# Performance work log

Hardware: AMD Instinct MI355X
Metric: run time of the kernel (lower is better)

The kernel has to match this reference:

```python
import jax, jax.numpy as jnp
import numpy as np

B, H, W = 64, 256, 256
G = 64
V = G * G          # 4096
HID = 512
S = 50


def _conv(x, w, b):
    # x: (B,C,H,W), w: (O,I,3,3) -> 'same' conv, NCHW
    y = jax.lax.conv_general_dilated(x, w, (1, 1), 'SAME',
                                     dimension_numbers=('NCHW', 'OIHW', 'NCHW'))
    return y + b[None, :, None, None]


def setup_inputs() -> dict:
    key = jax.random.key(0)
    ks = jax.random.split(key, 14)

    def lin(k, shape, fan_in):
        return (jax.random.normal(k, shape, jnp.float32) / np.float32(np.sqrt(fan_in)))

    return {
        'mask': jax.random.uniform(ks[0], (B, 1, H, W), jnp.float32),
        'target_ids': jax.random.randint(ks[1], (B, S), 0, V),
        'conv1_w': lin(ks[2], (16, 1, 3, 3), 9), 'conv1_b': jnp.zeros((16,), jnp.float32),
        'conv2_w': lin(ks[3], (32, 16, 3, 3), 16 * 9), 'conv2_b': jnp.zeros((32,), jnp.float32),
        'feat_w': lin(ks[4], (HID, 32), 32), 'feat_b': jnp.zeros((HID,), jnp.float32),
        'ctx_w': lin(ks[5], (HID, HID), HID), 'ctx_b': jnp.zeros((HID,), jnp.float32),
        'tok_emb': jax.random.normal(ks[6], (V + 1, HID), jnp.float32) * 0.02,
        'w_ih': lin(ks[7], (4 * HID, HID), HID), 'w_hh': lin(ks[8], (4 * HID, HID), HID),
        'b_ih': jnp.zeros((4 * HID,), jnp.float32), 'b_hh': jnp.zeros((4 * HID,), jnp.float32),
        'head_w': lin(ks[9], (V, HID), HID), 'head_b': jnp.zeros((V,), jnp.float32),
    }


def reference(mask, target_ids, conv1_w, conv1_b, conv2_w, conv2_b,
              feat_w, feat_b, ctx_w, ctx_b, tok_emb,
              w_ih, w_hh, b_ih, b_hh, head_w, head_b):
    b = mask.shape[0]
    vocab = head_w.shape[0]

    # --- CNN encoder ---
    x = jax.nn.relu(_conv(mask, conv1_w, conv1_b))                    # (B,16,H,W)
    x = jax.lax.reduce_window(x, -jnp.inf, jax.lax.max,
                              (1, 1, 2, 2), (1, 1, 2, 2), 'VALID')    # (B,16,H/2,W/2)
    x = jax.nn.relu(_conv(x, conv2_w, conv2_b))                       # (B,32,H/2,W/2)
    x = x.mean(axis=(2, 3))                                           # AdaptiveAvgPool2d(1) -> (B,32)

    h0 = x @ feat_w.T + feat_b                                        # (B,HID)
    c0 = jnp.zeros_like(h0)
    ctx = h0 @ ctx_w.T + ctx_b                                        # (B,HID)

    # Full teacher forcing (ratio=1.0): input token at t=0 is start token V,
    # at t>0 it is target_ids[:, t-1]. All embeddings gathered upfront.
    start = jnp.full((b, 1), vocab, dtype=target_ids.dtype)
    toks = jnp.concatenate([start, target_ids[:, :-1]], axis=1)       # (B,S)
    embs = tok_emb[toks]                                              # (B,S,HID)
    lstm_in = jnp.swapaxes(embs, 0, 1) + ctx[None]                    # (S,B,HID)

    bias = b_ih + b_hh

    def step(carry, inp):
        h, c = carry
        gates = inp @ w_ih.T + h @ w_hh.T + bias                      # (B,4*HID)
        i, f, g, o = jnp.split(gates, 4, axis=-1)
        c = jax.nn.sigmoid(f) * c + jax.nn.sigmoid(i) * jnp.tanh(g)
        h = jax.nn.sigmoid(o) * jnp.tanh(c)
        logit = h @ head_w.T + head_b                                 # (B,V)
        return (h, c), logit

    _, logits = jax.lax.scan(step, (h0, c0), lstm_in)                 # (S,B,V)
    return jnp.swapaxes(logits, 0, 1)                                 # (B,S,V)
```

## Files before the change

kernel.cpp:

```cpp
#include <hip/hip_runtime.h>
#include <cmath>

typedef __attribute__((ext_vector_type(8))) _Float16 f16x8;
typedef __attribute__((ext_vector_type(4))) float f32x4;
typedef __attribute__((ext_vector_type(4))) unsigned u32x4;

#define LSTM_NB 32

__device__ __forceinline__ unsigned short f2h(float x) {
  return __builtin_bit_cast(unsigned short, (_Float16)x);
}

__device__ __forceinline__ void gload16(const void* g, void* l) {
  __builtin_amdgcn_global_load_lds(
      (const __attribute__((address_space(1))) void*)g,
      (__attribute__((address_space(3))) void*)l, 16, 0, 0);
}

__device__ __forceinline__ void cload16(const void* p, u32x4* dst) {
  asm volatile("global_load_dwordx4 %0, %1, off sc0 sc1"
               : "=v"(*dst)
               : "v"(p));
}

__global__ __launch_bounds__(512) void k_conv(
    const float* __restrict__ mask, const float* __restrict__ w1,
    const float* __restrict__ b1, const float* __restrict__ w2,
    const float* __restrict__ b2, float* __restrict__ part)
{
  __shared__ float s_p1[16][18 * 36];
  __shared__ float s_w1[144];
  __shared__ float s_b1[16];
  __shared__ float s_w2[4608];
  __shared__ float s_b2[32];

  const int tid = threadIdx.x;
  const int b = blockIdx.x >> 5;
  const int tile = blockIdx.x & 31;
  const int px0 = (tile & 3) * 32, py0 = (tile >> 2) * 16;
  const float* mb = mask + (size_t)b * 65536;

  for (int i = tid; i < 144; i += 512) s_w1[i] = w1[i];
  for (int i = tid; i < 4608; i += 512) s_w2[i] = w2[i];
  if (tid < 16) s_b1[tid] = b1[tid];
  if (tid < 32) s_b2[tid] = b2[tid];
  __syncthreads();

  for (int idx = tid; idx < 18 * 34; idx += 512) {
    int ly = idx / 34, lx = idx - ly * 34;
    int py = py0 - 1 + ly, px = px0 - 1 + lx;
    if (py < 0 || py >= 128 || px < 0 || px >= 128) {
      for (int o = 0; o < 16; o++) s_p1[o][ly * 36 + lx] = 0.f;
    } else {
      float patch[4][4];
      int gy0 = 2 * py - 1, gx0 = 2 * px - 1;
#pragma unroll
      for (int i = 0; i < 4; i++) {
        int gy = gy0 + i;
        bool yok = (gy >= 0 && gy < 256);
#pragma unroll
        for (int j = 0; j < 4; j++) {
          int gx = gx0 + j;
          patch[i][j] = (yok && gx >= 0 && gx < 256) ? mb[gy * 256 + gx] : 0.f;
        }
      }
      for (int o = 0; o < 16; o++) {
        float m = 0.f;
#pragma unroll
        for (int dy = 0; dy < 2; dy++)
#pragma unroll
          for (int dx = 0; dx < 2; dx++) {
            float v = s_b1[o];
#pragma unroll
            for (int ky = 0; ky < 3; ky++)
#pragma unroll
              for (int kx = 0; kx < 3; kx++)
                v = fmaf(patch[dy + ky][dx + kx], s_w1[o * 9 + ky * 3 + kx], v);
            m = fmaxf(m, v);
          }
        s_p1[o][ly * 36 + lx] = m;
      }
    }
  }
  __syncthreads();

  const int ocg = tid >> 6;
  const int sp = tid & 63;
  const int sx = (sp & 7) * 4, sy = (sp >> 3) * 2;
  float acc[4][8];
#pragma unroll
  for (int a = 0; a < 4; a++)
#pragma unroll
    for (int q = 0; q < 8; q++) acc[a][q] = 0.f;

  for (int ic = 0; ic < 16; ic++) {
    float p[4][6];
#pragma unroll
    for (int i = 0; i < 4; i++) {
      const float* row = &s_p1[ic][(sy + i) * 36 + sx];
#pragma unroll
      for (int j = 0; j < 6; j++) p[i][j] = row[j];
    }
#pragma unroll
    for (int o4 = 0; o4 < 4; o4++) {
      const int oc = ocg * 4 + o4;
      const float* w = &s_w2[(oc * 16 + ic) * 9];
      float w00 = w[0], w01 = w[1], w02 = w[2];
      float w10 = w[3], w11 = w[4], w12 = w[5];
      float w20 = w[6], w21 = w[7], w22 = w[8];
#pragma unroll
      for (int y = 0; y < 2; y++)
#pragma unroll
        for (int x = 0; x < 4; x++) {
          float s = acc[o4][y * 4 + x];
          s = fmaf(p[y][x], w00, s);
          s = fmaf(p[y][x + 1], w01, s);
          s = fmaf(p[y][x + 2], w02, s);
          s = fmaf(p[y + 1][x], w10, s);
          s = fmaf(p[y + 1][x + 1], w11, s);
          s = fmaf(p[y + 1][x + 2], w12, s);
          s = fmaf(p[y + 2][x], w20, s);
          s = fmaf(p[y + 2][x + 1], w21, s);
          s = fmaf(p[y + 2][x + 2], w22, s);
          acc[o4][y * 4 + x] = s;
        }
    }
  }

  const int lane = tid & 63;
#pragma unroll
  for (int o4 = 0; o4 < 4; o4++) {
    float bv = s_b2[ocg * 4 + o4];
    float s = 0.f;
#pragma unroll
    for (int q = 0; q < 8; q++) s += fmaxf(acc[o4][q] + bv, 0.f);
    for (int off = 32; off > 0; off >>= 1) s += __shfl_down(s, off, 64);
    if (lane == 0) part[(b * 32 + tile) * 32 + ocg * 4 + o4] = s;
  }
}

__global__ __launch_bounds__(256) void k_pool_h0(
    const float* __restrict__ part, const float* __restrict__ feat_w,
    const float* __restrict__ feat_b, float* __restrict__ h0,
    unsigned short* __restrict__ h0f)
{
  const int b = blockIdx.x, tid = threadIdx.x;
  __shared__ float pl[32];
  if (tid < 32) {
    float s = 0.f;
    for (int t = 0; t < 32; t++) s += part[(b * 32 + t) * 32 + tid];
    pl[tid] = s * (1.0f / 16384.0f);
  }
  __syncthreads();
  for (int j = tid; j < 512; j += 256) {
    float acc = feat_b[j];
    const float* w = feat_w + j * 32;
#pragma unroll
    for (int ic = 0; ic < 32; ic++) acc = fmaf(pl[ic], w[ic], acc);
    h0[b * 512 + j] = acc;
    h0f[b * 512 + j] = f2h(acc);
  }
}

__global__ __launch_bounds__(256) void k_ctx(
    const float* __restrict__ h0, const float* __restrict__ ctx_w,
    const float* __restrict__ ctx_b, float* __restrict__ ctx)
{
  const int b = blockIdx.x, tid = threadIdx.x;
  __shared__ float hs[512];
  for (int k = tid; k < 512; k += 256) hs[k] = h0[b * 512 + k];
  __syncthreads();
  for (int j = tid; j < 512; j += 256) {
    const float* w = ctx_w + (size_t)j * 512;
    float s0 = 0.f, s1 = 0.f, s2 = 0.f, s3 = 0.f;
    for (int k = 0; k < 512; k += 4) {
      float4 w4 = *(const float4*)(w + k);
      s0 = fmaf(hs[k], w4.x, s0);
      s1 = fmaf(hs[k + 1], w4.y, s1);
      s2 = fmaf(hs[k + 2], w4.z, s2);
      s3 = fmaf(hs[k + 3], w4.w, s3);
    }
    ctx[b * 512 + j] = ctx_b[j] + ((s0 + s1) + (s2 + s3));
  }
}

__global__ __launch_bounds__(256) void k_f2h(
    const float* __restrict__ in, unsigned short* __restrict__ out, int n)
{
  int i = (blockIdx.x * 256 + threadIdx.x) * 4;
  if (i < n) {
    float4 v = *(const float4*)(in + i);
    unsigned lo = (unsigned)f2h(v.x) | ((unsigned)f2h(v.y) << 16);
    unsigned hi = (unsigned)f2h(v.z) | ((unsigned)f2h(v.w) << 16);
    *(uint2*)(out + i) = make_uint2(lo, hi);
  }
}

__global__ __launch_bounds__(64) void k_zero(int* __restrict__ p) {
  p[threadIdx.x] = 0;
}
__global__ __launch_bounds__(256) void k_zero_f(float* __restrict__ p) {
  p[blockIdx.x * 256 + threadIdx.x] = 0.f;
}

__global__ __launch_bounds__(128) void k_build_A(
    const float* __restrict__ tok_emb, const int* __restrict__ tgt,
    const float* __restrict__ ctx, unsigned short* __restrict__ A)
{
  const int r = blockIdx.x;
  const int t = r >> 6, b = r & 63;
  const int tok = (t == 0) ? 4096 : tgt[b * 50 + (t - 1)];
  const int i = threadIdx.x * 4;
  float4 ev = *(const float4*)(tok_emb + (size_t)tok * 512 + i);
  float4 cv = *(const float4*)(ctx + b * 512 + i);
  unsigned lo = (unsigned)f2h(ev.x + cv.x) | ((unsigned)f2h(ev.y + cv.y) << 16);
  unsigned hi = (unsigned)f2h(ev.z + cv.z) | ((unsigned)f2h(ev.w + cv.w) << 16);
  *(uint2*)(A + (size_t)r * 512 + i) = make_uint2(lo, hi);
}

template <int MODE>
__global__ __launch_bounds__(256) void k_gemm_mfma(
    const unsigned short* __restrict__ A, const unsigned short* __restrict__ B,
    const float* __restrict__ bias_a, const float* __restrict__ bias_b,
    float* __restrict__ C, int NB)
{
  __shared__ unsigned short sA[128 * 32];
  __shared__ unsigned short sB[128 * 32];
  const int tid = threadIdx.x;
  const int bx = blockIdx.x % NB, by = blockIdx.x / NB;
  const int lane = tid & 63, wv = tid >> 6;
  const int wr = wv >> 1, wc = wv & 1;
  const unsigned short* Ab = A + (size_t)by * 128 * 512;
  const unsigned short* Bb = B + (size_t)bx * 128 * 512;

  f32x4 acc[4][4];
#pragma unroll
  for (int m = 0; m < 4; m++)
#pragma unroll
    for (int n = 0; n < 4; n++) acc[m][n] = (f32x4){0.f, 0.f, 0.f, 0.f};

  const int r0 = tid >> 2, c0 = (tid & 3) * 8;
  const int idx1 = tid + 256;
  const int r1 = idx1 >> 2, c1 = (idx1 & 3) * 8;
  unsigned short* lA0 = sA + (size_t)wv * 512;
  unsigned short* lA1 = sA + 2048 + (size_t)wv * 512;
  unsigned short* lB0 = sB + (size_t)wv * 512;
  unsigned short* lB1 = sB + 2048 + (size_t)wv * 512;

  const int frow = lane & 15;
  const int foff = (lane >> 4) * 8;

  for (int kc = 0; kc < 512; kc += 32) {
    gload16(Ab + (size_t)r0 * 512 + kc + c0, lA0);
    gload16(Ab + (size_t)r1 * 512 + kc + c1, lA1);
    gload16(Bb + (size_t)r0 * 512 + kc + c0, lB0);
    gload16(Bb + (size_t)r1 * 512 + kc + c1, lB1);
    __syncthreads();

    f16x8 af[4], bfr[4];
#pragma unroll
    for (int m = 0; m < 4; m++)
      af[m] = *(const f16x8*)(sA + (wr * 64 + m * 16 + frow) * 32 + foff);
#pragma unroll
    for (int n = 0; n < 4; n++)
      bfr[n] = *(const f16x8*)(sB + (wc * 64 + n * 16 + frow) * 32 + foff);
#pragma unroll
    for (int m = 0; m < 4; m++)
#pragma unroll
      for (int n = 0; n < 4; n++)
        acc[m][n] = __builtin_amdgcn_mfma_f32_16x16x32_f16(
            af[m], bfr[n], acc[m][n], 0, 0, 0);
    __syncthreads();
  }

#pragma unroll
  for (int n = 0; n < 4; n++) {
    const int gc = bx * 128 + wc * 64 + n * 16 + (lane & 15);
    const float bv = (MODE == 0) ? (bias_a[gc] + bias_b[gc]) : bias_a[gc];
#pragma unroll
    for (int m = 0; m < 4; m++) {
      const int rb = by * 128 + wr * 64 + m * 16 + (lane >> 4) * 4;
#pragma unroll
      for (int j = 0; j < 4; j++) {
        const int r = rb + j;
        float v = acc[m][n][j] + bv;
        int t = r >> 6, bb = r & 63;
        if (MODE == 0) {
          C[(size_t)t * 131072 + (size_t)gc * 64 + bb] = v;
        } else {
          C[((size_t)bb * 50 + t) * 4096 + gc] = v;
        }
      }
    }
  }
}

__global__ __launch_bounds__(256, 1) void k_lstm_mfma(
    const float* __restrict__ xgT,
    const float* __restrict__ w_hh,
    const unsigned short* __restrict__ h0f,
    unsigned short* __restrict__ hallf,
    int* __restrict__ cnt)
{
  __shared__ unsigned short s_h[64 * 512];
  __shared__ float s_g[4][64][17];
  const int tid = threadIdx.x;
  const int kb = blockIdx.x;
  const int g = tid >> 6;
  const int lane = tid & 63;
  const int frow = lane & 15;
  const int foff = (lane >> 4) * 8;

  f16x8 wf[16];
  {
    const float* wrow = w_hh + (size_t)(g * 512 + kb * 16 + frow) * 512;
#pragma unroll
    for (int kf = 0; kf < 16; kf++) {
      float tmp[8];
      *(float4*)tmp = *(const float4*)(wrow + kf * 32 + foff);
      *(float4*)(tmp + 4) = *(const float4*)(wrow + kf * 32 + foff + 4);
#pragma unroll
      for (int j = 0; j < 8; j++) wf[kf][j] = (_Float16)tmp[j];
    }
  }

  float c[4] = {0.f, 0.f, 0.f, 0.f};
  const int b2 = tid & 63, dd2 = tid >> 6;

  for (int t = 0; t < 50; ++t) {
    const unsigned short* H = t ? hallf + (size_t)(t - 1) * 32768 : h0f;

    const float* xr =
        xgT + (size_t)t * 131072 + (size_t)(kb * 16 + dd2 * 4) * 64 + b2;
    float xv[16];
#pragma unroll
    for (int gq = 0; gq < 4; gq++)
#pragma unroll
      for (int i = 0; i < 4; i++)
        xv[gq * 4 + i] = xr[(size_t)(gq * 512 + i) * 64];

    {
      u32x4 r[16];
#pragma unroll
      for (int i = 0; i < 16; i++)
        cload16((const char*)H + (size_t)(tid + i * 256) * 16, &r[i]);
      asm volatile("s_waitcnt vmcnt(0)" ::: "memory");
      __builtin_amdgcn_sched_barrier(0);
#pragma unroll
      for (int i = 0; i < 16; i++) {
        int byte = (tid + i * 256) * 16;
        int swz = byte ^ (((byte >> 10) & 7) << 4);
        *(u32x4*)((char*)s_h + swz) = r[i];
      }
    }
    __syncthreads();

    f32x4 acc[4];
#pragma unroll
    for (int mt = 0; mt < 4; mt++) acc[mt] = (f32x4){0.f, 0.f, 0.f, 0.f};
#pragma unroll
    for (int kf = 0; kf < 16; kf++) {
#pragma unroll
      for (int mt = 0; mt < 4; mt++) {
        const int row = mt * 16 + frow;
        const int byte = (row << 10) + kf * 64 + foff * 2;
        const int swz = byte ^ ((row & 7) << 4);
        f16x8 ah = *(const f16x8*)((const char*)s_h + swz);
        acc[mt] =
            __builtin_amdgcn_mfma_f32_16x16x32_f16(ah, wf[kf], acc[mt], 0, 0, 0);
      }
    }
#pragma unroll
    for (int mt = 0; mt < 4; mt++)
#pragma unroll
      for (int j = 0; j < 4; j++)
        s_g[g][mt * 16 + (lane >> 4) * 4 + j][frow] = acc[mt][j];
    __syncthreads();

    unsigned long long qf = 0;
#pragma unroll
    for (int i = 0; i < 4; i++) {
      float gi = s_g[0][b2][dd2 * 4 + i] + xv[0 + i];
      float gf = s_g[1][b2][dd2 * 4 + i] + xv[4 + i];
      float gg = s_g[2][b2][dd2 * 4 + i] + xv[8 + i];
      float go = s_g[3][b2][dd2 * 4 + i] + xv[12 + i];
      float ig = 1.f / (1.f + expf(-gi));
      float fg = 1.f / (1.f + expf(-gf));
      float og = 1.f / (1.f + expf(-go));
      float gt = tanhf(gg);
      c[i] = fmaf(fg, c[i], ig * gt);
      float h = og * tanhf(c[i]);
      qf |= (unsigned long long)f2h(h) << (16 * i);
    }
    const size_t ho = (size_t)b2 * 512 + kb * 16 + dd2 * 4;
    __hip_atomic_store((unsigned long long*)(hallf + (size_t)t * 32768 + ho),
                       qf, __ATOMIC_RELAXED, __HIP_MEMORY_SCOPE_AGENT);
    __syncthreads();
    if (tid == 0) {
      __hip_atomic_fetch_add(&cnt[t], 1, __ATOMIC_RELAXED,
                             __HIP_MEMORY_SCOPE_AGENT);
      while (__hip_atomic_load(&cnt[t], __ATOMIC_RELAXED,
                               __HIP_MEMORY_SCOPE_AGENT) < LSTM_NB) {
        __builtin_amdgcn_s_sleep(1);
      }
    }
    __syncthreads();
  }
}

__global__ __launch_bounds__(256) void k_lstm_step1(
    const float* __restrict__ xgT, const float* __restrict__ w_hh,
    const float* __restrict__ hin, float* __restrict__ hout,
    unsigned short* __restrict__ hallf_t, float* __restrict__ cbuf, int t)
{
  __shared__ float s_w[8][512];
  __shared__ float s_g[2][4][64];
  const int tid = threadIdx.x;
  const int dd0 = blockIdx.x * 2;

  for (int idx = tid; idx < 1024; idx += 256) {
    int row = idx >> 7;
    int k4 = (idx & 127) << 2;
    int q_ = row >> 1, dd_i = row & 1;
    *(float4*)&s_w[row][k4] =
        *(const float4*)(w_hh + (size_t)(q_ * 512 + dd0 + dd_i) * 512 + k4);
  }
  const int b = tid & 63;
  const int q = tid >> 6;
  __syncthreads();

  const float* hc = hin + b * 512;
  const float* xr = xgT + (size_t)t * 131072 + (size_t)(q * 512 + dd0) * 64 + b;
  float a0 = xr[0], a1 = xr[64];
  const float* w0 = s_w[q * 2 + 0];
  const float* w1 = s_w[q * 2 + 1];
#pragma unroll 8
  for (int k = 0; k < 512; k += 4) {
    float4 h4 = *(const float4*)(hc + k);
    float4 u = *(const float4*)(w0 + k);
    float4 v = *(const float4*)(w1 + k);
    a0 = fmaf(h4.x, u.x, fmaf(h4.y, u.y, fmaf(h4.z, u.z, fmaf(h4.w, u.w, a0))));
    a1 = fmaf(h4.x, v.x, fmaf(h4.y, v.y, fmaf(h4.z, v.z, fmaf(h4.w, v.w, a1))));
  }
  s_g[0][q][b] = a0;
  s_g[1][q][b] = a1;
  __syncthreads();
  if (q < 2) {
    const int dd = dd0 + q;
    float gi = s_g[q][0][b], gf = s_g[q][1][b];
    float gg = s_g[q][2][b], go = s_g[q][3][b];
    float ig = 1.f / (1.f + expf(-gi));
    float fg = 1.f / (1.f + expf(-gf));
    float og = 1.f / (1.f + expf(-go));
    float gt = tanhf(gg);
    float c = fmaf(fg, cbuf[b * 512 + dd], ig * gt);
    float h = og * tanhf(c);
    cbuf[b * 512 + dd] = c;
    hout[b * 512 + dd] = h;
    hallf_t[(size_t)b * 512 + dd] = f2h(h);
  }
}

extern "C" void kernel_launch(void* const* d_in, const int* in_sizes, int n_in,
                              void* d_out, int out_size, void* d_ws,
                              size_t ws_size, hipStream_t stream) {
  const float* mask   = (const float*)d_in[0];
  const int*   tgt    = (const int*)d_in[1];
  const float* w1     = (const float*)d_in[2];
  const float* b1     = (const float*)d_in[3];
  const float* w2     = (const float*)d_in[4];
  const float* b2     = (const float*)d_in[5];
  const float* feat_w = (const float*)d_in[6];
  const float* feat_b = (const float*)d_in[7];
  const float* ctx_w  = (const float*)d_in[8];
  const float* ctx_b  = (const float*)d_in[9];
  const float* temb   = (const float*)d_in[10];
  const float* w_ih   = (const float*)d_in[11];
  const float* w_hh_p = (const float*)d_in[12];
  const float* b_ih   = (const float*)d_in[13];
  const float* b_hh   = (const float*)d_in[14];
  const float* head_w = (const float*)d_in[15];
  const float* head_b = (const float*)d_in[16];

  float* ws = (float*)d_ws;
  float* part  = ws;
  float* hbuf  = ws + 65536;
  float* ctx   = ws + 131072;
  int*   cnt   = (int*)(ws + 163840);
  unsigned short* h0f  = (unsigned short*)(ws + 163904);
  unsigned short* Ab16 = (unsigned short*)(ws + 180288);
  unsigned short* hallf = Ab16;
  unsigned short* wihb = (unsigned short*)(ws + 999488);
  unsigned short* hwb  = (unsigned short*)(ws + 1523776);
  float* xgT   = ws + 2572352;
  float* cbuf  = part;
  float* out   = (float*)d_out;

  k_conv<<<2048, 512, 0, stream>>>(mask, w1, b1, w2, b2, part);
  k_f2h<<<1024, 256, 0, stream>>>(w_ih, wihb, 1048576);
  k_f2h<<<2048, 256, 0, stream>>>(head_w, hwb, 2097152);
  k_zero<<<1, 64, 0, stream>>>(cnt);
  k_pool_h0<<<64, 256, 0, stream>>>(part, feat_w, feat_b, hbuf, h0f);
  k_ctx<<<64, 256, 0, stream>>>(hbuf, ctx_w, ctx_b, ctx);
  k_build_A<<<3200, 128, 0, stream>>>(temb, tgt, ctx, Ab16);
  k_gemm_mfma<0><<<25 * 16, 256, 0, stream>>>(Ab16, wihb, b_ih, b_hh, xgT, 16);

  {
    const float* xgT_c = xgT;
    const float* whh_c = w_hh_p;
    const unsigned short* h0f_c = h0f;
    unsigned short* hallf_c = hallf;
    int* cnt_c = cnt;
    void* args[] = {(void*)&xgT_c, (void*)&whh_c, (void*)&h0f_c,
                    (void*)&hallf_c, (void*)&cnt_c};
    hipError_t e = hipLaunchCooperativeKernel(
        (const void*)k_lstm_mfma, dim3(LSTM_NB), dim3(256), args, 0, stream);
    if (e != hipSuccess) {
      (void)hipGetLastError();
      k_zero_f<<<128, 256, 0, stream>>>(cbuf);
      for (int t = 0; t < 50; t++) {
        const float* hin = hbuf + (t & 1) * 32768;
        float* hout = hbuf + ((t + 1) & 1) * 32768;
        k_lstm_step1<<<256, 256, 0, stream>>>(
            xgT, w_hh_p, hin, hout, hallf + (size_t)t * 32768, cbuf, t);
      }
    }
  }

  k_gemm_mfma<1><<<25 * 32, 256, 0, stream>>>(hallf, hwb, head_b, nullptr, out, 32);
}
```

Measured before the change: 568.3 us.

## Fuse vocab head projection into persistent LSTM kernel to overlap with recurrence

Extends the cooperative LSTM kernel with 192 extra blocks that compute the output-head GEMM for each timestep as soon as that step's hidden state is published. The shared counter barrier becomes per-block flags, so head blocks can wait on a specific step and recurrence blocks skip the wait at the last step. This overlaps the head projection with the serial recurrence instead of running it as a separate GEMM afterwards. The risks are head blocks competing for CUs and memory bandwidth with the latency-critical recurrent blocks, and a larger cooperative grid that must fit co-resident.

```diff
diff --git a/kernel.cpp b/kernel.cpp
--- a/kernel.cpp
+++ b/kernel.cpp
@@ -5,7 +5,8 @@
 typedef __attribute__((ext_vector_type(4))) float f32x4;
 typedef __attribute__((ext_vector_type(4))) unsigned u32x4;
 
-#define LSTM_NB 32
+#define REC_NB 32
+#define HEAD_NB 192
 
 __device__ __forceinline__ unsigned short f2h(float x) {
   return __builtin_bit_cast(unsigned short, (_Float16)x);
@@ -196,8 +197,9 @@
   }
 }
 
-__global__ __launch_bounds__(64) void k_zero(int* __restrict__ p) {
-  p[threadIdx.x] = 0;
+__global__ __launch_bounds__(256) void k_zero_i(int* __restrict__ p, int n) {
+  int i = blockIdx.x * 256 + threadIdx.x;
+  if (i < n) p[i] = 0;
 }
 __global__ __launch_bounds__(256) void k_zero_f(float* __restrict__ p) {
   p[blockIdx.x * 256 + threadIdx.x] = 0.f;
@@ -295,116 +297,190 @@
   }
 }
 
-__global__ __launch_bounds__(256, 1) void k_lstm_mfma(
+__global__ __launch_bounds__(256, 1) void k_lstm_head(
     const float* __restrict__ xgT,
     const float* __restrict__ w_hh,
     const unsigned short* __restrict__ h0f,
     unsigned short* __restrict__ hallf,
-    int* __restrict__ cnt)
+    const unsigned short* __restrict__ hwb,
+    const float* __restrict__ head_b,
+    float* __restrict__ out,
+    int* __restrict__ flags)
 {
   __shared__ unsigned short s_h[64 * 512];
   __shared__ float s_g[4][64][17];
   const int tid = threadIdx.x;
-  const int kb = blockIdx.x;
-  const int g = tid >> 6;
   const int lane = tid & 63;
   const int frow = lane & 15;
   const int foff = (lane >> 4) * 8;
 
-  f16x8 wf[16];
-  {
-    const float* wrow = w_hh + (size_t)(g * 512 + kb * 16 + frow) * 512;
-#pragma unroll
-    for (int kf = 0; kf < 16; kf++) {
-      float tmp[8];
-      *(float4*)tmp = *(const float4*)(wrow + kf * 32 + foff);
-      *(float4*)(tmp + 4) = *(const float4*)(wrow + kf * 32 + foff + 4);
-#pragma unroll
-      for (int j = 0; j < 8; j++) wf[kf][j] = (_Float16)tmp[j];
-    }
-  }
-
-  float c[4] = {0.f, 0.f, 0.f, 0.f};
-  const int b2 = tid & 63, dd2 = tid >> 6;
-
-  for (int t = 0; t < 50; ++t) {
-    const unsigned short* H = t ? hallf + (size_t)(t - 1) * 32768 : h0f;
-
-    const float* xr =
-        xgT + (size_t)t * 131072 + (size_t)(kb * 16 + dd2 * 4) * 64 + b2;
-    float xv[16];
-#pragma unroll
-    for (int gq = 0; gq < 4; gq++)
-#pragma unroll
-      for (int i = 0; i < 4; i++)
-        xv[gq * 4 + i] = xr[(size_t)(gq * 512 + i) * 64];
-
+  if (blockIdx.x < REC_NB) {
+    const int kb = blockIdx.x;
+    const int g = tid >> 6;
+
+    f16x8 wf[16];
     {
-      u32x4 r[16];
-#pragma unroll
-      for (int i = 0; i < 16; i++)
-        cload16((const char*)H + (size_t)(tid + i * 256) * 16, &r[i]);
-      asm volatile("s_waitcnt vmcnt(0)" ::: "memory");
-      __builtin_amdgcn_sched_barrier(0);
-#pragma unroll
-      for (int i = 0; i < 16; i++) {
-        int byte = (tid + i * 256) * 16;
-        int swz = byte ^ (((byte >> 10) & 7) << 4);
-        *(u32x4*)((char*)s_h + swz) = r[i];
-      }
-    }
-    __syncthreads();
-
-    f32x4 acc[4];
-#pragma unroll
-    for (int mt = 0; mt < 4; mt++) acc[mt] = (f32x4){0.f, 0.f, 0.f, 0.f};
-#pragma unroll
-    for (int kf = 0; kf < 16; kf++) {
-#pragma unroll
-      for (int mt = 0; mt < 4; mt++) {
-        const int row = mt * 16 + frow;
-        const int byte = (row << 10) + kf * 64 + foff * 2;
-        const int swz = byte ^ ((row & 7) << 4);
-        f16x8 ah = *(const f16x8*)((const char*)s_h + swz);
-        acc[mt] =
-            __builtin_amdgcn_mfma_f32_16x16x32_f16(ah, wf[kf], acc[mt], 0, 0, 0);
-      }
-    }
-#pragma unroll
-    for (int mt = 0; mt < 4; mt++)
-#pragma unroll
-      for (int j = 0; j < 4; j++)
-        s_g[g][mt * 16 + (lane >> 4) * 4 + j][frow] = acc[mt][j];
-    __syncthreads();
-
-    unsigned long long qf = 0;
-#pragma unroll
-    for (int i = 0; i < 4; i++) {
-      float gi = s_g[0][b2][dd2 * 4 + i] + xv[0 + i];
-      float gf = s_g[1][b2][dd2 * 4 + i] + xv[4 + i];
-      float gg = s_g[2][b2][dd2 * 4 + i] + xv[8 + i];
-      float go = s_g[3][b2][dd2 * 4 + i] + xv[12 + i];
-      float ig = 1.f / (1.f + expf(-gi));
-      float fg = 1.f / (1.f + expf(-gf));
-      float og = 1.f / (1.f + expf(-go));
-      float gt = tanhf(gg);
-      c[i] = fmaf(fg, c[i], ig * gt);
-      float h = og * tanhf(c[i]);
-      qf |= (unsigned long long)f2h(h) << (16 * i);
-    }
-    const size_t ho = (size_t)b2 * 512 + kb * 16 + dd2 * 4;
-    __hip_atomic_store((unsigned long long*)(hallf + (size_t)t * 32768 + ho),
-                       qf, __ATOMIC_RELAXED, __HIP_MEMORY_SCOPE_AGENT);
-    __syncthreads();
-    if (tid == 0) {
-      __hip_atomic_fetch_add(&cnt[t], 1, __ATOMIC_RELAXED,
-                             __HIP_MEMORY_SCOPE_AGENT);
-      while (__hip_atomic_load(&cnt[t], __ATOMIC_RELAXED,
-                               __HIP_MEMORY_SCOPE_AGENT) < LSTM_NB) {
-        __builtin_amdgcn_s_sleep(1);
-      }
-    }
-    __syncthreads();
+      const float* wrow = w_hh + (size_t)(g * 512 + kb * 16 + frow) * 512;
+#pragma unroll
+      for (int kf = 0; kf < 16; kf++) {
+        float tmp[8];
+        *(float4*)tmp = *(const float4*)(wrow + kf * 32 + foff);
+        *(float4*)(tmp + 4) = *(const float4*)(wrow + kf * 32 + foff + 4);
+#pragma unroll
+        for (int j = 0; j < 8; j++) wf[kf][j] = (_Float16)tmp[j];
+      }
+    }
+
+    float c[4] = {0.f, 0.f, 0.f, 0.f};
+    const int b2 = tid & 63, dd2 = tid >> 6;
+
+    for (int t = 0; t < 50; ++t) {
+      const unsigned short* H = t ? hallf + (size_t)(t - 1) * 32768 : h0f;
+
+      const float* xr =
+          xgT + (size_t)t * 131072 + (size_t)(kb * 16 + dd2 * 4) * 64 + b2;
+      float xv[16];
+#pragma unroll
+      for (int gq = 0; gq < 4; gq++)
+#pragma unroll
+        for (int i = 0; i < 4; i++)
+          xv[gq * 4 + i] = xr[(size_t)(gq * 512 + i) * 64];
+
+      {
+        u32x4 r[16];
+#pragma unroll
+        for (int i = 0; i < 16; i++)
+          cload16((const char*)H + (size_t)(tid + i * 256) * 16, &r[i]);
+        asm volatile("s_waitcnt vmcnt(0)" ::: "memory");
+        __builtin_amdgcn_sched_barrier(0);
+#pragma unroll
+        for (int i = 0; i < 16; i++) {
+          int byte = (tid + i * 256) * 16;
+          int swz = byte ^ (((byte >> 10) & 7) << 4);
+          *(u32x4*)((char*)s_h + swz) = r[i];
+        }
+      }
+      __syncthreads();
+
+      f32x4 acc[4];
+#pragma unroll
+      for (int mt = 0; mt < 4; mt++) acc[mt] = (f32x4){0.f, 0.f, 0.f, 0.f};
+#pragma unroll
+      for (int kf = 0; kf < 16; kf++) {
+#pragma unroll
+        for (int mt = 0; mt < 4; mt++) {
+          const int row = mt * 16 + frow;
+          const int byte = (row << 10) + kf * 64 + foff * 2;
+          const int swz = byte ^ ((row & 7) << 4);
+          f16x8 ah = *(const f16x8*)((const char*)s_h + swz);
+          acc[mt] = __builtin_amdgcn_mfma_f32_16x16x32_f16(ah, wf[kf],
+                                                           acc[mt], 0, 0, 0);
+        }
+      }
+#pragma unroll
+      for (int mt = 0; mt < 4; mt++)
+#pragma unroll
+        for (int j = 0; j < 4; j++)
+          s_g[g][mt * 16 + (lane >> 4) * 4 + j][frow] = acc[mt][j];
+      __syncthreads();
+
+      unsigned long long qf = 0;
+#pragma unroll
+      for (int i = 0; i < 4; i++) {
+        float gi = s_g[0][b2][dd2 * 4 + i] + xv[0 + i];
+        float gf = s_g[1][b2][dd2 * 4 + i] + xv[4 + i];
+        float gg = s_g[2][b2][dd2 * 4 + i] + xv[8 + i];
+        float go = s_g[3][b2][dd2 * 4 + i] + xv[12 + i];
+        float ig = 1.f / (1.f + expf(-gi));
+        float fg = 1.f / (1.f + expf(-gf));
+        float og = 1.f / (1.f + expf(-go));
+        float gt = tanhf(gg);
+        c[i] = fmaf(fg, c[i], ig * gt);
+        float h = og * tanhf(c[i]);
+        qf |= (unsigned long long)f2h(h) << (16 * i);
+      }
+      const size_t ho = (size_t)b2 * 512 + kb * 16 + dd2 * 4;
+      __hip_atomic_store((unsigned long long*)(hallf + (size_t)t * 32768 + ho),
+                         qf, __ATOMIC_RELAXED, __HIP_MEMORY_SCOPE_AGENT);
+      __syncthreads();
+
+      if (tid == 0)
+        __hip_atomic_store(&flags[t * 32 + kb], 1, __ATOMIC_RELAXED,
+                           __HIP_MEMORY_SCOPE_AGENT);
+      if (t < 49 && tid < 32) {
+        while (__hip_atomic_load(&flags[t * 32 + tid], __ATOMIC_RELAXED,
+                                 __HIP_MEMORY_SCOPE_AGENT) == 0) {
+          __builtin_amdgcn_s_sleep(1);
+        }
+      }
+      __syncthreads();
+    }
+  } else {
+    const int hb = blockIdx.x - REC_NB;
+    const int ct = hb % 64;
+    const int tg = hb / 64;
+    const int wv = tid >> 6;
+
+    f16x8 bf[16];
+    const unsigned short* brow =
+        hwb + (size_t)(ct * 64 + wv * 16 + frow) * 512;
+#pragma unroll
+    for (int kf = 0; kf < 16; kf++)
+      bf[kf] = *(const f16x8*)(brow + kf * 32 + foff);
+    const float bias = head_b[ct * 64 + wv * 16 + frow];
+
+    for (int t = tg; t < 50; t += 3) {
+      if (tid < 32) {
+        while (__hip_atomic_load(&flags[t * 32 + tid], __ATOMIC_RELAXED,
+                                 __HIP_MEMORY_SCOPE_AGENT) == 0) {
+          __builtin_amdgcn_s_sleep(1);
+        }
+      }
+      __syncthreads();
+
+      {
+        const char* src = (const char*)(hallf + (size_t)t * 32768);
+        u32x4 r[16];
+#pragma unroll
+        for (int i = 0; i < 16; i++)
+          cload16(src + (size_t)(tid + i * 256) * 16, &r[i]);
+        asm volatile("s_waitcnt vmcnt(0)" ::: "memory");
+        __builtin_amdgcn_sched_barrier(0);
+#pragma unroll
+        for (int i = 0; i < 16; i++) {
+          int byte = (tid + i * 256) * 16;
+          int swz = byte ^ (((byte >> 10) & 7) << 4);
+          *(u32x4*)((char*)s_h + swz) = r[i];
+        }
+      }
+      __syncthreads();
+
+      f32x4 acc[4];
+#pragma unroll
+      for (int m = 0; m < 4; m++) acc[m] = (f32x4){0.f, 0.f, 0.f, 0.f};
+#pragma unroll
+      for (int kf = 0; kf < 16; kf++) {
+#pragma unroll
+        for (int m = 0; m < 4; m++) {
+          const int row = m * 16 + frow;
+          const int byte = (row << 10) + kf * 64 + foff * 2;
+          const int swz = byte ^ ((row & 7) << 4);
+          f16x8 ah = *(const f16x8*)((const char*)s_h + swz);
+          acc[m] = __builtin_amdgcn_mfma_f32_16x16x32_f16(ah, bf[kf], acc[m],
+                                                          0, 0, 0);
+        }
+      }
+      const int gc = ct * 64 + wv * 16 + (lane & 15);
+#pragma unroll
+      for (int m = 0; m < 4; m++) {
+#pragma unroll
+        for (int j = 0; j < 4; j++) {
+          const int b = m * 16 + (lane >> 4) * 4 + j;
+          out[((size_t)b * 50 + t) * 4096 + gc] = acc[m][j] + bias;
+        }
+      }
+      __syncthreads();
+    }
   }
 }
 
@@ -486,20 +562,20 @@
   float* part  = ws;
   float* hbuf  = ws + 65536;
   float* ctx   = ws + 131072;
-  int*   cnt   = (int*)(ws + 163840);
-  unsigned short* h0f  = (unsigned short*)(ws + 163904);
-  unsigned short* Ab16 = (unsigned short*)(ws + 180288);
+  int*   flags = (int*)(ws + 163840);
+  unsigned short* h0f  = (unsigned short*)(ws + 165440);
+  unsigned short* Ab16 = (unsigned short*)(ws + 181824);
   unsigned short* hallf = Ab16;
-  unsigned short* wihb = (unsigned short*)(ws + 999488);
-  unsigned short* hwb  = (unsigned short*)(ws + 1523776);
-  float* xgT   = ws + 2572352;
+  unsigned short* wihb = (unsigned short*)(ws + 1001024);
+  unsigned short* hwb  = (unsigned short*)(ws + 1525312);
+  float* xgT   = ws + 2573888;
   float* cbuf  = part;
   float* out   = (float*)d_out;
 
   k_conv<<<2048, 512, 0, stream>>>(mask, w1, b1, w2, b2, part);
   k_f2h<<<1024, 256, 0, stream>>>(w_ih, wihb, 1048576);
   k_f2h<<<2048, 256, 0, stream>>>(head_w, hwb, 2097152);
-  k_zero<<<1, 64, 0, stream>>>(cnt);
+  k_zero_i<<<7, 256, 0, stream>>>(flags, 1600);
   k_pool_h0<<<64, 256, 0, stream>>>(part, feat_w, feat_b, hbuf, h0f);
   k_ctx<<<64, 256, 0, stream>>>(hbuf, ctx_w, ctx_b, ctx);
   k_build_A<<<3200, 128, 0, stream>>>(temb, tgt, ctx, Ab16);
@@ -510,11 +586,16 @@
     const float* whh_c = w_hh_p;
     const unsigned short* h0f_c = h0f;
     unsigned short* hallf_c = hallf;
-    int* cnt_c = cnt;
-    void* args[] = {(void*)&xgT_c, (void*)&whh_c, (void*)&h0f_c,
-                    (void*)&hallf_c, (void*)&cnt_c};
+    const unsigned short* hwb_c = hwb;
+    const float* headb_c = head_b;
+    float* out_c = out;
+    int* flags_c = flags;
+    void* args[] = {(void*)&xgT_c,  (void*)&whh_c,   (void*)&h0f_c,
+                    (void*)&hallf_c, (void*)&hwb_c,  (void*)&headb_c,
+                    (void*)&out_c,   (void*)&flags_c};
     hipError_t e = hipLaunchCooperativeKernel(
-        (const void*)k_lstm_mfma, dim3(LSTM_NB), dim3(256), args, 0, stream);
+        (const void*)k_lstm_head, dim3(REC_NB + HEAD_NB), dim3(256), args, 0,
+        stream);
     if (e != hipSuccess) {
       (void)hipGetLastError();
       k_zero_f<<<128, 256, 0, stream>>>(cbuf);
@@ -524,8 +605,8 @@
         k_lstm_step1<<<256, 256, 0, stream>>>(
             xgT, w_hh_p, hin, hout, hallf + (size_t)t * 32768, cbuf, t);
       }
-    }
-  }
-
-  k_gemm_mfma<1><<<25 * 32, 256, 0, stream>>>(hallf, hwb, head_b, nullptr, out, 32);
-}
+      k_gemm_mfma<1><<<25 * 32, 256, 0, stream>>>(hallf, hwb, head_b, nullptr,
+                                                  out, 32);
+    }
+  }
+}
```

New measurement: 617.3 us. 8.6% more time.
